# Kernel tuning notes

Hardware: AMD Instinct MI355X
Metric: run time of the kernel (lower is better)

Reference implementation:

```python
import jax, jax.numpy as jnp
import numpy as np
from jax import lax

B = 16384
BN_EPS = 1e-5


def setup_inputs() -> dict:
    key = jax.random.key(0)
    ks = jax.random.split(key, 6)
    x = jax.random.normal(ks[0], (B, 1, 28, 28), jnp.float32)
    conv_w = jax.random.normal(ks[1], (4, 1, 3, 3), jnp.float32) * 0.2
    bn_gamma = jnp.ones((4,), jnp.float32)
    bn_beta = jnp.zeros((4,), jnp.float32)
    bn_mean = jnp.zeros((4,), jnp.float32)
    bn_var = jnp.ones((4,), jnp.float32)
    var_params = jax.random.normal(ks[2], (4,), jnp.float32)
    lin_w = jax.random.normal(ks[3], (10, 784), jnp.float32) * 0.03
    lin_b = jnp.zeros((10,), jnp.float32)
    return {"x": x, "conv_w": conv_w, "bn_gamma": bn_gamma, "bn_beta": bn_beta,
            "bn_mean": bn_mean, "bn_var": bn_var, "var_params": var_params,
            "lin_w": lin_w, "lin_b": lin_b}


def _ry_w0(s, theta):
    # apply RY(theta) to wire 0 (axis -2) of real state s[..., 2, 2]
    c, si = jnp.cos(theta * 0.5), jnp.sin(theta * 0.5)
    R = jnp.stack([jnp.stack([c, -si]), jnp.stack([si, c])])
    return jnp.einsum('ij,...jk->...ik', R, s)


def _ry_w1(s, theta):
    # apply RY(theta) to wire 1 (axis -1)
    c, si = jnp.cos(theta * 0.5), jnp.sin(theta * 0.5)
    R = jnp.stack([jnp.stack([c, -si]), jnp.stack([si, c])])
    return jnp.einsum('ij,...kj->...ki', R, s)


def _quantum_features(img, v):
    # img: [B, 28, 28] -> features [B, 196*4] (patch-major, 4 expvals each)
    b = img.shape[0]
    p = img.reshape(b, 14, 2, 14, 2).transpose(0, 1, 3, 2, 4)  # [B,14,14,2,2]
    # encoding RYs on same wire compose: angles a = p0+p2 (wire0), b = p1+p3 (wire1)
    ha = (p[..., 0, 0] + p[..., 1, 0]) * 0.5
    hb = (p[..., 0, 1] + p[..., 1, 1]) * 0.5
    w0 = jnp.stack([jnp.cos(ha), jnp.sin(ha)], axis=-1)
    w1 = jnp.stack([jnp.cos(hb), jnp.sin(hb)], axis=-1)
    s = w0[..., :, None] * w1[..., None, :]  # real statevector [B,14,14,2,2]
    # CNOT(control=0, target=1): flip wire1 where wire0 == 1
    s = jnp.stack([s[..., 0, :], s[..., 1, ::-1]], axis=-2)
    s = _ry_w0(s, v[0])
    s = _ry_w1(s, v[1])
    # CNOT(control=1, target=0): flip wire0 where wire1 == 1
    s = jnp.stack([s[..., :, 0], s[..., ::-1, 1]], axis=-1)
    s = _ry_w0(s, v[2])
    s = _ry_w1(s, v[3])
    z0 = jnp.sum(s[..., 0, :] ** 2 - s[..., 1, :] ** 2, axis=-1)
    z1 = jnp.sum(s[..., :, 0] ** 2 - s[..., :, 1] ** 2, axis=-1)
    x0 = 2.0 * jnp.sum(s[..., 0, :] * s[..., 1, :], axis=-1)
    x1 = 2.0 * jnp.sum(s[..., :, 0] * s[..., :, 1], axis=-1)
    return jnp.stack([z0, z1, x0, x1], axis=-1).reshape(b, -1)  # [B,784]


def reference(x, conv_w, bn_gamma, bn_beta, bn_mean, bn_var, var_params, lin_w, lin_b):
    b = x.shape[0]
    # classical branch: conv(s=2,p=1) -> BN (eval) -> ReLU -> flatten
    h = lax.conv_general_dilated(x, conv_w, window_strides=(2, 2),
                                 padding=((1, 1), (1, 1)))  # [B,4,14,14]
    inv = bn_gamma / jnp.sqrt(bn_var + BN_EPS)
    h = h * inv[None, :, None, None] + (bn_beta - bn_mean * inv)[None, :, None, None]
    h = jnp.maximum(h, 0.0)
    cls_out = h.reshape(b, -1)  # [B,784]
    # quantum branch over 2x2 patches
    q_out = _quantum_features(x[:, 0], var_params)  # [B,784]
    fused = cls_out + q_out
    logits = fused @ lin_w.T + lin_b
    return jax.nn.log_softmax(logits, axis=-1)
```

## Files before the change

### kernel.cpp

```cpp
#include <hip/hip_runtime.h>
#include <math.h>


typedef __fp16 h2 __attribute__((ext_vector_type(2)));
typedef __fp16 h4 __attribute__((ext_vector_type(4)));
typedef __fp16 h8 __attribute__((ext_vector_type(8)));
typedef float f32x4 __attribute__((ext_vector_type(4)));

#define NSAMP 8
#define FSTRIDE 808

__device__ __forceinline__ float rfl(float v) {
    return __int_as_float(__builtin_amdgcn_readfirstlane(__float_as_int(v)));
}

__global__ __launch_bounds__(256, 6)
void quanv_fused(const float* __restrict__ x,
                 const float* __restrict__ conv_w,
                 const float* __restrict__ bn_gamma,
                 const float* __restrict__ bn_beta,
                 const float* __restrict__ bn_mean,
                 const float* __restrict__ bn_var,
                 const float* __restrict__ var_params,
                 const float* __restrict__ lin_w,
                 const float* __restrict__ lin_b,
                 float* __restrict__ out, int B)
{
    __shared__ __align__(16) __fp16 clsB[NSAMP * FSTRIDE];
    __shared__ __align__(16) __fp16 qB[NSAMP * FSTRIDE];

    const int tid  = threadIdx.x;
    const int lane = tid & 63;
    const int wave = tid >> 6;

    if (tid < 128) {
        int r = tid >> 4, buf = (tid >> 3) & 1, w = tid & 7;
        int* wp = (int*)((buf ? qB : clsB) + r * FSTRIDE + 784);
        wp[w] = 0;
    }

    const int bcol = lane & 15, bkg = lane >> 4;
    const __fp16 hz = (__fp16)0.f;
    const h8 hz8 = {hz, hz, hz, hz, hz, hz, hz, hz};
    h8 bfrag[7];
    #pragma unroll
    for (int t = 0; t < 7; ++t) {
        int st = wave * 7 + t;
        int kb = st * 32 + bkg * 8;
        h8 bf = hz8;
        if (bcol < 10 && kb < 784) {
            const float4* lw4 = (const float4*)(lin_w + bcol * 784 + kb);
            float4 v0 = lw4[0], v1 = lw4[1];
            h2 p0 = __builtin_amdgcn_cvt_pkrtz(v0.x, v0.y);
            h2 p1 = __builtin_amdgcn_cvt_pkrtz(v0.z, v0.w);
            h2 p2 = __builtin_amdgcn_cvt_pkrtz(v1.x, v1.y);
            h2 p3 = __builtin_amdgcn_cvt_pkrtz(v1.z, v1.w);
            h8 tv = {p0.x, p0.y, p1.x, p1.y, p2.x, p2.y, p3.x, p3.y};
            bf = tv;
        }
        bfrag[t] = bf;
    }

    float inv[4], addc[4];
    #pragma unroll
    for (int c = 0; c < 4; ++c) {
        float iv = bn_gamma[c] * rsqrtf(bn_var[c] + 1e-5f);
        inv[c]  = rfl(iv);
        addc[c] = rfl(bn_beta[c] - bn_mean[c] * iv);
    }
    float cv[4], sv[4];
    #pragma unroll
    for (int k = 0; k < 4; ++k) {
        float s, c;
        __sincosf(var_params[k] * 0.5f, &s, &c);
        sv[k] = rfl(s); cv[k] = rfl(c);
    }

    const int s_loc = tid >> 5;
    const int q32   = tid & 31;
    const int sg    = blockIdx.x * NSAMP + s_loc;
    const int sgc   = (sg < B) ? sg : (B - 1);
    const float* xs = x + (size_t)sgc * 784;
    __fp16* clsRow  = clsB + s_loc * FSTRIDE;
    __fp16* qRow    = qB   + s_loc * FSTRIDE;

    #pragma unroll
    for (int it = 0; it < 7; ++it) {
        int p = q32 + 32 * it;
        if (p < 196) {
            unsigned ii = (unsigned)p / 14u;
            int j  = p - (int)ii * 14;
            int om = (int)ii * 56 + 2 * j;

            float2 Rm = *(const float2*)(xs + om);
            float2 Rb = *(const float2*)(xs + om + 28);
            int ot = om - 28;  ot  = (ot  > 0) ? ot  : 0;
            float2 Rt = *(const float2*)(xs + ot);
            int olt = om - 30; olt = (olt > 0) ? olt : 0;
            float2 Lt = *(const float2*)(xs + olt);
            int olm = om - 2;  olm = (olm > 0) ? olm : 0;
            float2 Lm = *(const float2*)(xs + olm);
            float2 Lb = *(const float2*)(xs + olm + 28);

            float mt = (ii > 0u) ? 1.f : 0.f;
            float ml = (j  > 0 ) ? 1.f : 0.f;
            float a00 = Lt.y * (mt * ml), a01 = Rt.x * mt, a02 = Rt.y * mt;
            float a10 = Lm.y * ml,        a11 = Rm.x,      a12 = Rm.y;
            float a20 = Lb.y * ml,        a21 = Rb.x,      a22 = Rb.y;

            #pragma unroll
            for (int c = 0; c < 4; ++c) {
                float h = conv_w[c*9+0]*a00 + conv_w[c*9+1]*a01 + conv_w[c*9+2]*a02
                        + conv_w[c*9+3]*a10 + conv_w[c*9+4]*a11 + conv_w[c*9+5]*a12
                        + conv_w[c*9+6]*a20 + conv_w[c*9+7]*a21 + conv_w[c*9+8]*a22;
                h = h * inv[c] + addc[c];
                clsRow[c * 196 + p] = (__fp16)fmaxf(h, 0.f);
            }

            float ha = 0.5f * (a11 + a21);
            float hb = 0.5f * (a12 + a22);
            float c0, s0, c1, s1;
            __sincosf(ha, &s0, &c0);
            __sincosf(hb, &s1, &c1);
            float m00 = c0*c1, m01 = c0*s1;
            float m10 = s0*s1, m11 = s0*c1;
            float t00 = cv[0]*m00 - sv[0]*m10, t01 = cv[0]*m01 - sv[0]*m11;
            float t10 = sv[0]*m00 + cv[0]*m10, t11 = sv[0]*m01 + cv[0]*m11;
            float u00 = cv[1]*t00 - sv[1]*t01, u01 = sv[1]*t00 + cv[1]*t01;
            float u10 = cv[1]*t10 - sv[1]*t11, u11 = sv[1]*t10 + cv[1]*t11;
            float tmp = u01; u01 = u11; u11 = tmp;
            float p00 = cv[2]*u00 - sv[2]*u10, p01 = cv[2]*u01 - sv[2]*u11;
            float p10 = sv[2]*u00 + cv[2]*u10, p11 = sv[2]*u01 + cv[2]*u11;
            float q00 = cv[3]*p00 - sv[3]*p01, q01 = sv[3]*p00 + cv[3]*p01;
            float q10 = cv[3]*p10 - sv[3]*p11, q11 = sv[3]*p10 + cv[3]*p11;

            float z0 = q00*q00 + q01*q01 - q10*q10 - q11*q11;
            float z1 = q00*q00 + q10*q10 - q01*q01 - q11*q11;
            float x0 = 2.f * (q00*q10 + q01*q11);
            float x1 = 2.f * (q00*q01 + q10*q11);
            h2 zz = __builtin_amdgcn_cvt_pkrtz(z0, z1);
            h2 xx = __builtin_amdgcn_cvt_pkrtz(x0, x1);
            h4 qv = {zz.x, zz.y, xx.x, xx.y};
            *(h4*)(qRow + 4 * p) = qv;
        }
    }

    __syncthreads();

    f32x4 acc = {0.f, 0.f, 0.f, 0.f};
    {
        const int arow = lane & 15, akg = lane >> 4;
        #pragma unroll
        for (int t = 0; t < 7; ++t) {
            int st = wave * 7 + t;
            if (st < 25) {
                h8 a = hz8;
                if (arow < NSAMP) {
                    int off = arow * FSTRIDE + st * 32 + akg * 8;
                    a = *(const h8*)(clsB + off) + *(const h8*)(qB + off);
                }
                acc = __builtin_amdgcn_mfma_f32_16x16x32_f16(a, bfrag[t], acc, 0, 0, 0);
            }
        }
    }

    __syncthreads();
    float* pw = (float*)clsB;
    if (lane < 32) {
        const int col = lane & 15, rb = (lane >> 4) * 4;
        #pragma unroll
        for (int r = 0; r < 4; ++r)
            pw[(wave * 8 + rb + r) * 16 + col] = acc[r];
    }
    __syncthreads();

    if (tid < 128) {
        const int c  = tid & 15;
        const int sl = tid >> 4;
        float L = pw[sl * 16 + c] + pw[(8 + sl) * 16 + c]
                + pw[(16 + sl) * 16 + c] + pw[(24 + sl) * 16 + c];
        L = (c < 10) ? (L + lin_b[c]) : -1e30f;
        float mx = L;
        mx = fmaxf(mx, __shfl_xor(mx, 1, 16));
        mx = fmaxf(mx, __shfl_xor(mx, 2, 16));
        mx = fmaxf(mx, __shfl_xor(mx, 4, 16));
        mx = fmaxf(mx, __shfl_xor(mx, 8, 16));
        float se = (c < 10) ? __expf(L - mx) : 0.f;
        se += __shfl_xor(se, 1, 16);
        se += __shfl_xor(se, 2, 16);
        se += __shfl_xor(se, 4, 16);
        se += __shfl_xor(se, 8, 16);
        const int sg2 = blockIdx.x * NSAMP + sl;
        if (c < 10 && sg2 < B)
            out[(size_t)sg2 * 10 + c] = L - mx - __logf(se);
    }
}

extern "C" void kernel_launch(void* const* d_in, const int* in_sizes, int n_in,
                              void* d_out, int out_size, void* d_ws, size_t ws_size,
                              hipStream_t stream) {
    const float* x          = (const float*)d_in[0];
    const float* conv_w     = (const float*)d_in[1];
    const float* bn_gamma   = (const float*)d_in[2];
    const float* bn_beta    = (const float*)d_in[3];
    const float* bn_mean    = (const float*)d_in[4];
    const float* bn_var     = (const float*)d_in[5];
    const float* var_params = (const float*)d_in[6];
    const float* lin_w      = (const float*)d_in[7];
    const float* lin_b      = (const float*)d_in[8];
    float* out = (float*)d_out;

    const int B = in_sizes[0] / 784;
    const int blocks = (B + NSAMP - 1) / NSAMP;
    quanv_fused<<<blocks, 256, 0, stream>>>(x, conv_w, bn_gamma, bn_beta, bn_mean,
                                            bn_var, var_params, lin_w, lin_b, out, B);
}
```

Measured before the change: 110.8 us.

## Stage input images into LDS with coalesced float4 loads before compute

The block's 8 images are now loaded with fully coalesced float4 global reads into LDS, replacing the scattered float2 global gathers per patch. Conv and quantum features are computed from LDS into registers, then written to the feature buffers after a barrier, since those buffers alias the staging area. The register arrays and extra barrier raise register pressure, so the occupancy hint drops from 6 to 4 blocks per CU, which may reduce latency hiding.

```diff
diff --git a/kernel.cpp b/kernel.cpp
--- a/kernel.cpp
+++ b/kernel.cpp
@@ -14,7 +14,7 @@
     return __int_as_float(__builtin_amdgcn_readfirstlane(__float_as_int(v)));
 }
 
-__global__ __launch_bounds__(256, 6)
+__global__ __launch_bounds__(256, 4)
 void quanv_fused(const float* __restrict__ x,
                  const float* __restrict__ conv_w,
                  const float* __restrict__ bn_gamma,
@@ -26,17 +26,29 @@
                  const float* __restrict__ lin_b,
                  float* __restrict__ out, int B)
 {
-    __shared__ __align__(16) __fp16 clsB[NSAMP * FSTRIDE];
-    __shared__ __align__(16) __fp16 qB[NSAMP * FSTRIDE];
+    __shared__ __align__(16) unsigned char lds_raw[2 * NSAMP * FSTRIDE * 2];
+    __fp16* clsB = (__fp16*)lds_raw;
+    __fp16* qB   = (__fp16*)(lds_raw + NSAMP * FSTRIDE * 2);
 
     const int tid  = threadIdx.x;
     const int lane = tid & 63;
     const int wave = tid >> 6;
 
-    if (tid < 128) {
-        int r = tid >> 4, buf = (tid >> 3) & 1, w = tid & 7;
-        int* wp = (int*)((buf ? qB : clsB) + r * FSTRIDE + 784);
-        wp[w] = 0;
+    {
+        const int base4 = blockIdx.x * (NSAMP * 196);
+        const int maxg4 = B * 196 - 1;
+        float4 stg[7];
+        #pragma unroll
+        for (int t = 0; t < 7; ++t) {
+            int g = base4 + tid + 256 * t;
+            g = (g < maxg4) ? g : maxg4;
+            stg[t] = ((const float4*)x)[g];
+        }
+        #pragma unroll
+        for (int t = 0; t < 7; ++t) {
+            int idx = tid + 256 * t;
+            if (idx < NSAMP * 196) ((float4*)lds_raw)[idx] = stg[t];
+        }
     }
 
     const int bcol = lane & 15, bkg = lane >> 4;
@@ -76,72 +88,97 @@
         sv[k] = rfl(s); cv[k] = rfl(c);
     }
 
+    __syncthreads();
+
     const int s_loc = tid >> 5;
     const int q32   = tid & 31;
-    const int sg    = blockIdx.x * NSAMP + s_loc;
-    const int sgc   = (sg < B) ? sg : (B - 1);
-    const float* xs = x + (size_t)sgc * 784;
-    __fp16* clsRow  = clsB + s_loc * FSTRIDE;
-    __fp16* qRow    = qB   + s_loc * FSTRIDE;
-
+    const float* imgS = (const float*)lds_raw + s_loc * 784;
+
+    h4 clsr[7], qr[7];
+    #pragma unroll
+    for (int it = 0; it < 7; ++it) {
+        int p  = q32 + 32 * it;
+        int pc = (p < 196) ? p : 195;
+        unsigned ii = (unsigned)pc / 14u;
+        int j  = pc - (int)ii * 14;
+        int rm = (int)ii * 56 + 2 * j;
+
+        float2 Rm = *(const float2*)(imgS + rm);
+        float2 Rb = *(const float2*)(imgS + rm + 28);
+        int rt = rm - 28; rt = (rt > 0) ? rt : 0;
+        float2 Rt = *(const float2*)(imgS + rt);
+        int cl = rm - 1;  cl = (cl > 0) ? cl : 0;
+        float a10 = imgS[cl];
+        float a20 = imgS[cl + 28];
+        int ct = cl - 28; ct = (ct > 0) ? ct : 0;
+        float a00 = imgS[ct];
+
+        float mt = (ii > 0u) ? 1.f : 0.f;
+        float ml = (j  > 0 ) ? 1.f : 0.f;
+        a00 *= mt * ml;
+        float a01 = Rt.x * mt, a02 = Rt.y * mt;
+        a10 *= ml;
+        float a11 = Rm.x, a12 = Rm.y;
+        a20 *= ml;
+        float a21 = Rb.x, a22 = Rb.y;
+
+        float hc[4];
+        #pragma unroll
+        for (int c = 0; c < 4; ++c) {
+            float h = conv_w[c*9+0]*a00 + conv_w[c*9+1]*a01 + conv_w[c*9+2]*a02
+                    + conv_w[c*9+3]*a10 + conv_w[c*9+4]*a11 + conv_w[c*9+5]*a12
+                    + conv_w[c*9+6]*a20 + conv_w[c*9+7]*a21 + conv_w[c*9+8]*a22;
+            hc[c] = fmaxf(h * inv[c] + addc[c], 0.f);
+        }
+        h2 ca = __builtin_amdgcn_cvt_pkrtz(hc[0], hc[1]);
+        h2 cb = __builtin_amdgcn_cvt_pkrtz(hc[2], hc[3]);
+        h4 cq = {ca.x, ca.y, cb.x, cb.y};
+        clsr[it] = cq;
+
+        float ha = 0.5f * (a11 + a21);
+        float hb = 0.5f * (a12 + a22);
+        float c0, s0, c1, s1;
+        __sincosf(ha, &s0, &c0);
+        __sincosf(hb, &s1, &c1);
+        float m00 = c0*c1, m01 = c0*s1;
+        float m10 = s0*s1, m11 = s0*c1;
+        float t00 = cv[0]*m00 - sv[0]*m10, t01 = cv[0]*m01 - sv[0]*m11;
+        float t10 = sv[0]*m00 + cv[0]*m10, t11 = sv[0]*m01 + cv[0]*m11;
+        float u00 = cv[1]*t00 - sv[1]*t01, u01 = sv[1]*t00 + cv[1]*t01;
+        float u10 = cv[1]*t10 - sv[1]*t11, u11 = sv[1]*t10 + cv[1]*t11;
+        float tmp = u01; u01 = u11; u11 = tmp;
+        float p00 = cv[2]*u00 - sv[2]*u10, p01 = cv[2]*u01 - sv[2]*u11;
+        float p10 = sv[2]*u00 + cv[2]*u10, p11 = sv[2]*u01 + cv[2]*u11;
+        float q00 = cv[3]*p00 - sv[3]*p01, q01 = sv[3]*p00 + cv[3]*p01;
+        float q10 = cv[3]*p10 - sv[3]*p11, q11 = sv[3]*p10 + cv[3]*p11;
+
+        float z0 = q00*q00 + q01*q01 - q10*q10 - q11*q11;
+        float z1 = q00*q00 + q10*q10 - q01*q01 - q11*q11;
+        float x0 = 2.f * (q00*q10 + q01*q11);
+        float x1 = 2.f * (q00*q01 + q10*q11);
+        h2 zz = __builtin_amdgcn_cvt_pkrtz(z0, z1);
+        h2 xx = __builtin_amdgcn_cvt_pkrtz(x0, x1);
+        h4 qv = {zz.x, zz.y, xx.x, xx.y};
+        qr[it] = qv;
+    }
+
+    __syncthreads();
+
+    if (tid < 128) {
+        int r = tid >> 4, buf = (tid >> 3) & 1, w = tid & 7;
+        int* wp = (int*)((buf ? qB : clsB) + r * FSTRIDE + 784);
+        wp[w] = 0;
+    }
     #pragma unroll
     for (int it = 0; it < 7; ++it) {
         int p = q32 + 32 * it;
         if (p < 196) {
-            unsigned ii = (unsigned)p / 14u;
-            int j  = p - (int)ii * 14;
-            int om = (int)ii * 56 + 2 * j;
-
-            float2 Rm = *(const float2*)(xs + om);
-            float2 Rb = *(const float2*)(xs + om + 28);
-            int ot = om - 28;  ot  = (ot  > 0) ? ot  : 0;
-            float2 Rt = *(const float2*)(xs + ot);
-            int olt = om - 30; olt = (olt > 0) ? olt : 0;
-            float2 Lt = *(const float2*)(xs + olt);
-            int olm = om - 2;  olm = (olm > 0) ? olm : 0;
-            float2 Lm = *(const float2*)(xs + olm);
-            float2 Lb = *(const float2*)(xs + olm + 28);
-
-            float mt = (ii > 0u) ? 1.f : 0.f;
-            float ml = (j  > 0 ) ? 1.f : 0.f;
-            float a00 = Lt.y * (mt * ml), a01 = Rt.x * mt, a02 = Rt.y * mt;
-            float a10 = Lm.y * ml,        a11 = Rm.x,      a12 = Rm.y;
-            float a20 = Lb.y * ml,        a21 = Rb.x,      a22 = Rb.y;
-
-            #pragma unroll
-            for (int c = 0; c < 4; ++c) {
-                float h = conv_w[c*9+0]*a00 + conv_w[c*9+1]*a01 + conv_w[c*9+2]*a02
-                        + conv_w[c*9+3]*a10 + conv_w[c*9+4]*a11 + conv_w[c*9+5]*a12
-                        + conv_w[c*9+6]*a20 + conv_w[c*9+7]*a21 + conv_w[c*9+8]*a22;
-                h = h * inv[c] + addc[c];
-                clsRow[c * 196 + p] = (__fp16)fmaxf(h, 0.f);
-            }
-
-            float ha = 0.5f * (a11 + a21);
-            float hb = 0.5f * (a12 + a22);
-            float c0, s0, c1, s1;
-            __sincosf(ha, &s0, &c0);
-            __sincosf(hb, &s1, &c1);
-            float m00 = c0*c1, m01 = c0*s1;
-            float m10 = s0*s1, m11 = s0*c1;
-            float t00 = cv[0]*m00 - sv[0]*m10, t01 = cv[0]*m01 - sv[0]*m11;
-            float t10 = sv[0]*m00 + cv[0]*m10, t11 = sv[0]*m01 + cv[0]*m11;
-            float u00 = cv[1]*t00 - sv[1]*t01, u01 = sv[1]*t00 + cv[1]*t01;
-            float u10 = cv[1]*t10 - sv[1]*t11, u11 = sv[1]*t10 + cv[1]*t11;
-            float tmp = u01; u01 = u11; u11 = tmp;
-            float p00 = cv[2]*u00 - sv[2]*u10, p01 = cv[2]*u01 - sv[2]*u11;
-            float p10 = sv[2]*u00 + cv[2]*u10, p11 = sv[2]*u01 + cv[2]*u11;
-            float q00 = cv[3]*p00 - sv[3]*p01, q01 = sv[3]*p00 + cv[3]*p01;
-            float q10 = cv[3]*p10 - sv[3]*p11, q11 = sv[3]*p10 + cv[3]*p11;
-
-            float z0 = q00*q00 + q01*q01 - q10*q10 - q11*q11;
-            float z1 = q00*q00 + q10*q10 - q01*q01 - q11*q11;
-            float x0 = 2.f * (q00*q10 + q01*q11);
-            float x1 = 2.f * (q00*q01 + q10*q11);
-            h2 zz = __builtin_amdgcn_cvt_pkrtz(z0, z1);
-            h2 xx = __builtin_amdgcn_cvt_pkrtz(x0, x1);
-            h4 qv = {zz.x, zz.y, xx.x, xx.y};
-            *(h4*)(qRow + 4 * p) = qv;
+            __fp16* cr = clsB + s_loc * FSTRIDE + p;
+            cr[0]   = clsr[it].x;
+            cr[196] = clsr[it].y;
+            cr[392] = clsr[it].z;
+            cr[588] = clsr[it].w;
+            *(h4*)(qB + s_loc * FSTRIDE + 4 * p) = qr[it];
         }
     }
 
```

New measurement: 113.5 us. +2.4%, slower.
